# Kernel tuning notes

Hardware: AMD Instinct MI355X
Metric: run time of the kernel (lower is better)

Reference implementation:

```python
import jax, jax.numpy as jnp
import numpy as np

# physics constants (match PDELoss defaults)
RHO, CP, VZ, KT = 0.3, 1200.0, 0.5, 0.06
# Arrhenius-style soot source constants (representative RadiationPINN.soot_source_terms)
A_NUC, E_NUC = 1.0e4, 2.0e4
A_GROW, E_GROW = 5.0e3, 1.2e4
A_OX, E_OX = 1.0e5, 1.6e4

N, IN_DIM, H, OUT, N_FUELS, EMB = 262144, 12, 128, 7, 4, 8


def mlp(X, emb_rows, W1, b1, W2, b2, W3, b3, Wo, bo):
    # X: (N,4) coords; emb_rows: (N,8) fuel embedding -> T (N,1), fv (N,1), Y (N,5)
    h = jnp.concatenate([X, emb_rows], axis=-1)
    h = jnp.tanh(h @ W1 + b1)
    h = jnp.tanh(h @ W2 + b2)
    h = jnp.tanh(h @ W3 + b3)
    o = h @ Wo + bo
    T = 300.0 + 2000.0 * jax.nn.sigmoid(o[:, 0:1])
    fv = jax.nn.softplus(o[:, 1:2]) * 1e-6
    Y = jax.nn.softmax(o[:, 2:7], axis=-1)
    return T, fv, Y


def soot_sources(T, Y_prec, Y_O2, fv):
    nuc = A_NUC * Y_prec * jnp.exp(-E_NUC / T)
    grow = A_GROW * Y_prec * fv * jnp.exp(-E_GROW / T)
    ox = A_OX * Y_O2 * fv * jnp.sqrt(T) * jnp.exp(-E_OX / T)
    return nuc, grow, ox


def pde_loss(inputs, fuel_ids, W1, b1, W2, b2, W3, b3, Wo, bo, emb):
    emb_rows = emb[fuel_ids]  # (N, EMB), constant w.r.t. inputs
    params = (W1, b1, W2, b2, W3, b3, Wo, bo)

    def T_of(X):
        return mlp(X, emb_rows, *params)[0]

    def fv_of(X):
        return mlp(X, emb_rows, *params)[1]

    n = inputs.shape[0]
    Ez = jnp.zeros_like(inputs).at[:, 1].set(1.0)  # direction d/dz
    Er = jnp.zeros_like(inputs).at[:, 2].set(1.0)  # direction d/dr

    # forward-mode (Taylor) derivatives: nested jvp gives 1st and 2nd order in one pass
    dT_dz_fn = lambda X: jax.jvp(T_of, (X,), (Ez,))[1]
    dT_dz, d2T_dz2 = jax.jvp(dT_dz_fn, (inputs,), (Ez,))
    dT_dr_fn = lambda X: jax.jvp(T_of, (X,), (Er,))[1]
    dT_dr, d2T_dr2 = jax.jvp(dT_dr_fn, (inputs,), (Er,))
    _, dfv_dz = jax.jvp(fv_of, (inputs,), (Ez,))

    T, fv, Y = mlp(inputs, emb_rows, *params)
    Y_prec, Y_O2 = Y[:, 3:4], Y[:, 4:5]

    r = inputs[:, 2:3]
    r_safe = jnp.maximum(r, 1e-6)
    laplacian_r = d2T_dr2 + dT_dr / r_safe
    energy_res = RHO * CP * VZ * dT_dz - KT * laplacian_r - KT * d2T_dz2

    nuc, grow, ox = soot_sources(T, Y_prec, Y_O2, fv)
    soot_res = VZ * dfv_dz - nuc - grow + ox

    loss_energy = jnp.mean(energy_res ** 2)
    loss_soot = jnp.mean(soot_res ** 2)
    return jnp.stack([loss_energy, loss_soot, loss_energy + loss_soot])


def setup_inputs() -> dict:
    key = jax.random.key(0)
    ks = jax.random.split(key, 12)
    inputs = jax.random.uniform(ks[0], (N, 4), dtype=jnp.float32)
    fuel_ids = jax.random.randint(ks[1], (N,), 0, N_FUELS)
    s1, sh, so = 1.0 / np.sqrt(IN_DIM), 1.0 / np.sqrt(H), 1.0 / np.sqrt(H)
    return {
        "inputs": inputs,
        "fuel_ids": fuel_ids,
        "W1": jax.random.normal(ks[2], (IN_DIM, H), jnp.float32) * s1,
        "b1": jnp.zeros((H,), jnp.float32),
        "W2": jax.random.normal(ks[3], (H, H), jnp.float32) * sh,
        "b2": jnp.zeros((H,), jnp.float32),
        "W3": jax.random.normal(ks[4], (H, H), jnp.float32) * sh,
        "b3": jnp.zeros((H,), jnp.float32),
        "Wo": jax.random.normal(ks[5], (H, OUT), jnp.float32) * so,
        "bo": jnp.zeros((OUT,), jnp.float32),
        "emb": jax.random.normal(ks[6], (N_FUELS, EMB), jnp.float32) * 0.1,
    }


def reference(inputs, fuel_ids, W1, b1, W2, b2, W3, b3, Wo, bo, emb):
    return pde_loss(inputs, fuel_ids, W1, b1, W2, b2, W3, b3, Wo, bo, emb)
```

## Files before the change

kernel.cpp:

```cpp
#include <hip/hip_runtime.h>
#include <math.h>

#define NPTS 262144
#define PTS  16
#define NBLK (NPTS / PTS)
#define AP   136

typedef _Float16 f16;
typedef f16    f16x4 __attribute__((ext_vector_type(4)));
typedef f16    f16x8 __attribute__((ext_vector_type(8)));
typedef __fp16 h16x2 __attribute__((ext_vector_type(2)));
typedef __fp16 h16x4 __attribute__((ext_vector_type(4)));
typedef float  f32x4 __attribute__((ext_vector_type(4)));


__device__ __forceinline__ h16x2 pk(float a, float b) {
    return __builtin_amdgcn_cvt_pkrtz(a, b);
}
__device__ __forceinline__ f16x4 mrg(h16x2 lo, h16x2 hi) {
    h16x4 v = __builtin_shufflevector(lo, hi, 0, 1, 2, 3);
    return __builtin_bit_cast(f16x4, v);
}

__device__ __forceinline__ float fast_tanh(float z) {
    float e = __expf(2.f * z);
    return 1.f - __fdividef(2.f, e + 1.f);
}

__global__ void prep_weights(const float* __restrict__ W1, const float* __restrict__ W2,
                             const float* __restrict__ W3, const float* __restrict__ Wo,
                             const float* __restrict__ bo,
                             f16* __restrict__ wt1, f16* __restrict__ wt2,
                             f16* __restrict__ wt3, f16* __restrict__ wot,
                             float* __restrict__ bot)
{
    int tid    = blockIdx.x * blockDim.x + threadIdx.x;
    int stride = gridDim.x * blockDim.x;
    for (int i = tid; i < 128 * 32; i += stride) {
        int k = i >> 7, n = i & 127;
        wt1[n * 32 + k] = (f16)((k < 12) ? W1[k * 128 + n] : 0.f);
    }
    for (int i = tid; i < 128 * 128; i += stride) {
        int k = i >> 7, n = i & 127;
        wt2[n * 128 + k] = (f16)W2[i];
        wt3[n * 128 + k] = (f16)W3[i];
    }
    for (int i = tid; i < 16 * 128; i += stride) {
        int k = i >> 4, n = i & 15;
        wot[n * 128 + k] = (f16)((n < 7) ? Wo[k * 7 + n] : 0.f);
    }
    if (tid < 16) bot[tid] = (tid < 7) ? bo[tid] : 0.f;
}

__device__ __forceinline__ void transform_store(
    f16 (*sAct)[PTS][AP], const f32x4 acc[5], const f32x4 bv,
    int pt, int n0q)
{
    float t[4], s[4];
#pragma unroll
    for (int r = 0; r < 4; ++r) {
        float z = acc[0][r] + bv[r];
        t[r] = fast_tanh(z);
        s[r] = 1.f - t[r] * t[r];
    }
    h16x2 T[2]  = { pk(t[0], t[1]), pk(t[2], t[3]) };
    h16x2 S[2]  = { pk(s[0], s[1]), pk(s[2], s[3]) };
    h16x2 A1[2] = { pk(acc[1][0], acc[1][1]), pk(acc[1][2], acc[1][3]) };
    h16x2 A2[2] = { pk(acc[2][0], acc[2][1]), pk(acc[2][2], acc[2][3]) };
    h16x2 A3[2] = { pk(acc[3][0], acc[3][1]), pk(acc[3][2], acc[3][3]) };
    h16x2 A4[2] = { pk(acc[4][0], acc[4][1]), pk(acc[4][2], acc[4][3]) };
    h16x2 TZ[2], TZZ[2], TR[2], TRR[2];
#pragma unroll
    for (int p = 0; p < 2; ++p) {
        h16x2 n2t = -(T[p] + T[p]);
        TZ[p]  = S[p] * A1[p];
        TR[p]  = S[p] * A3[p];
        TZZ[p] = n2t * (TZ[p] * A1[p]) + S[p] * A2[p];
        TRR[p] = n2t * (TR[p] * A3[p]) + S[p] * A4[p];
    }
    *(f16x4*)&sAct[0][pt][n0q] = mrg(T[0], T[1]);
    *(f16x4*)&sAct[1][pt][n0q] = mrg(TZ[0], TZ[1]);
    *(f16x4*)&sAct[2][pt][n0q] = mrg(TZZ[0], TZZ[1]);
    *(f16x4*)&sAct[3][pt][n0q] = mrg(TR[0], TR[1]);
    *(f16x4*)&sAct[4][pt][n0q] = mrg(TRR[0], TRR[1]);
}

__device__ __forceinline__ void layer128(
    f16 (*sAct)[PTS][AP], const f16* __restrict__ Wt, const float* __restrict__ b,
    int half, int q, int m)
{
    f16x8 Bv[5][4];
#pragma unroll
    for (int c = 0; c < 5; ++c)
#pragma unroll
        for (int kt = 0; kt < 4; ++kt)
            Bv[c][kt] = *(const f16x8*)&sAct[c][m][kt * 32 + q * 8];
    __syncthreads();

    const f32x4 z4 = {0.f, 0.f, 0.f, 0.f};
#pragma unroll
    for (int ct0 = 0; ct0 < 4; ++ct0) {
        const int n0 = (half * 4 + ct0) * 16;
        const f16* wp = &Wt[(n0 + m) * 128 + q * 8];
        f16x8 A0 = *(const f16x8*)(wp);
        f16x8 A1 = *(const f16x8*)(wp + 32);
        f16x8 A2 = *(const f16x8*)(wp + 64);
        f16x8 A3 = *(const f16x8*)(wp + 96);
        f32x4 bb = *(const f32x4*)&b[n0 + q * 4];
        f32x4 acc[5];
#pragma unroll
        for (int c = 0; c < 5; ++c) acc[c] = __builtin_amdgcn_mfma_f32_16x16x32_f16(A0, Bv[c][0], z4, 0, 0, 0);
#pragma unroll
        for (int c = 0; c < 5; ++c) acc[c] = __builtin_amdgcn_mfma_f32_16x16x32_f16(A1, Bv[c][1], acc[c], 0, 0, 0);
#pragma unroll
        for (int c = 0; c < 5; ++c) acc[c] = __builtin_amdgcn_mfma_f32_16x16x32_f16(A2, Bv[c][2], acc[c], 0, 0, 0);
#pragma unroll
        for (int c = 0; c < 5; ++c) acc[c] = __builtin_amdgcn_mfma_f32_16x16x32_f16(A3, Bv[c][3], acc[c], 0, 0, 0);

        transform_store(sAct, acc, bb, m, n0 + q * 4);
    }
    __syncthreads();
}

__global__ __launch_bounds__(128, 3) void pde_main(
    const float* __restrict__ X,
    const int*   __restrict__ fid,
    const float* __restrict__ emb,
    const float* __restrict__ b1, const float* __restrict__ b2,
    const float* __restrict__ b3,
    const f16* __restrict__ Wt1, const f16* __restrict__ Wt2,
    const f16* __restrict__ Wt3, const f16* __restrict__ Wot,
    const float* __restrict__ bot,
    float* __restrict__ partials)
{
    __shared__ f32x4 smem4[5 * PTS * AP * 2 / 16];
    __shared__ float sRes[PTS][2];
    f16   (*sAct)[PTS][AP] = (f16(*)[PTS][AP])smem4;
    float (*sO)[PTS][17]   = (float(*)[PTS][17])smem4;

    const int tid  = threadIdx.x;
    const int half = tid >> 6;
    const int lane = tid & 63;
    const int q    = lane >> 4;
    const int m    = lane & 15;
    const int p0   = blockIdx.x * PTS;

    for (int idx = tid; idx < 5 * PTS * 32; idx += 128) {
        int k = idx & 31;
        int p = (idx >> 5) & (PTS - 1);
        int c = idx >> 9;
        float v = 0.f;
        if (c == 0) {
            if (k < 4)       v = X[(p0 + p) * 4 + k];
            else if (k < 12) v = emb[fid[p0 + p] * 8 + (k - 4)];
        } else if (c == 1) { v = (k == 1) ? 1.f : 0.f; }
        else if (c == 3)   { v = (k == 2) ? 1.f : 0.f; }
        sAct[c][p][k] = (f16)v;
    }
    __syncthreads();

    {
        f16x8 Bv[5];
#pragma unroll
        for (int c = 0; c < 5; ++c)
            Bv[c] = *(const f16x8*)&sAct[c][m][q * 8];
        __syncthreads();
        const f32x4 z4 = {0.f, 0.f, 0.f, 0.f};
#pragma unroll
        for (int ct0 = 0; ct0 < 4; ++ct0) {
            const int n0 = (half * 4 + ct0) * 16;
            f16x8 A0 = *(const f16x8*)&Wt1[(n0 + m) * 32 + q * 8];
            f32x4 bb = *(const f32x4*)&b1[n0 + q * 4];
            f32x4 acc[5];
#pragma unroll
            for (int c = 0; c < 5; ++c)
                acc[c] = __builtin_amdgcn_mfma_f32_16x16x32_f16(A0, Bv[c], z4, 0, 0, 0);
            transform_store(sAct, acc, bb, m, n0 + q * 4);
        }
        __syncthreads();
    }

    layer128(sAct, Wt2, b2, half, q, m);
    layer128(sAct, Wt3, b3, half, q, m);

    f16x8 Bh[5][4];
    f32x4 boq = {0.f, 0.f, 0.f, 0.f};
    if (half == 0) {
#pragma unroll
        for (int c = 0; c < 5; ++c)
#pragma unroll
            for (int kt = 0; kt < 4; ++kt)
                Bh[c][kt] = *(const f16x8*)&sAct[c][m][kt * 32 + q * 8];
        boq = *(const f32x4*)&bot[q * 4];
    }
    __syncthreads();
    if (half == 0) {
        const f16* wp = &Wot[m * 128 + q * 8];
        f16x8 A0 = *(const f16x8*)(wp);
        f16x8 A1 = *(const f16x8*)(wp + 32);
        f16x8 A2 = *(const f16x8*)(wp + 64);
        f16x8 A3 = *(const f16x8*)(wp + 96);
        const f32x4 z4 = {0.f, 0.f, 0.f, 0.f};
        f32x4 acc[5];
#pragma unroll
        for (int c = 0; c < 5; ++c) acc[c] = __builtin_amdgcn_mfma_f32_16x16x32_f16(A0, Bh[c][0], z4, 0, 0, 0);
#pragma unroll
        for (int c = 0; c < 5; ++c) acc[c] = __builtin_amdgcn_mfma_f32_16x16x32_f16(A1, Bh[c][1], acc[c], 0, 0, 0);
#pragma unroll
        for (int c = 0; c < 5; ++c) acc[c] = __builtin_amdgcn_mfma_f32_16x16x32_f16(A2, Bh[c][2], acc[c], 0, 0, 0);
#pragma unroll
        for (int c = 0; c < 5; ++c) acc[c] = __builtin_amdgcn_mfma_f32_16x16x32_f16(A3, Bh[c][3], acc[c], 0, 0, 0);
#pragma unroll
        for (int c = 0; c < 5; ++c)
#pragma unroll
            for (int r = 0; r < 4; ++r)
                sO[c][m][q * 4 + r] = acc[c][r] + ((c == 0) ? boq[r] : 0.f);
    }
    __syncthreads();

    if (tid < PTS) {
        const int pt = tid;
        float o0   = sO[0][pt][0], o1  = sO[0][pt][1];
        float o0z  = sO[1][pt][0], o1z = sO[1][pt][1];
        float o0zz = sO[2][pt][0];
        float o0r  = sO[3][pt][0];
        float o0rr = sO[4][pt][0];

        float sg  = __fdividef(1.f, 1.f + __expf(-o0));
        float T   = 300.f + 2000.f * sg;
        float sp  = sg * (1.f - sg);
        float spp = sp * (1.f - 2.f * sg);
        float Tz  = 2000.f * sp * o0z;
        float Tzz = 2000.f * (spp * o0z * o0z + sp * o0zz);
        float Tr  = 2000.f * sp * o0r;
        float Trr = 2000.f * (spp * o0r * o0r + sp * o0rr);

        float fv  = ((o1 > 20.f) ? o1 : __logf(1.f + __expf(o1))) * 1e-6f;
        float s1  = __fdividef(1.f, 1.f + __expf(-o1));
        float fvz = s1 * o1z * 1e-6f;

        float y0 = sO[0][pt][2], y1 = sO[0][pt][3], y2 = sO[0][pt][4];
        float y3 = sO[0][pt][5], y4 = sO[0][pt][6];
        float mx = fmaxf(fmaxf(fmaxf(y0, y1), fmaxf(y2, y3)), y4);
        float e0 = __expf(y0 - mx), e1 = __expf(y1 - mx), e2 = __expf(y2 - mx);
        float e3 = __expf(y3 - mx), e4 = __expf(y4 - mx);
        float inv = __fdividef(1.f, e0 + e1 + e2 + e3 + e4);
        float Yp = e3 * inv;
        float Yo = e4 * inv;

        float r   = X[(p0 + pt) * 4 + 2];
        float rs  = fmaxf(r, 1e-6f);
        float rT  = __fdividef(1.f, T);
        float lap = Trr + __fdividef(Tr, rs);
        float eres = 180.f * Tz - 0.06f * lap - 0.06f * Tzz;

        float nuc  = 1e4f * Yp * __expf(-20000.f * rT);
        float grow = 5e3f * Yp * fv * __expf(-12000.f * rT);
        float ox   = 1e5f * Yo * fv * sqrtf(T) * __expf(-16000.f * rT);
        float sres = 0.5f * fvz - nuc - grow + ox;

        sRes[pt][0] = eres * eres;
        sRes[pt][1] = sres * sres;
    }
    __syncthreads();
    if (tid == 0) {
        float se = 0.f, ss = 0.f;
#pragma unroll
        for (int p = 0; p < PTS; ++p) { se += sRes[p][0]; ss += sRes[p][1]; }
        partials[2 * blockIdx.x]     = se;
        partials[2 * blockIdx.x + 1] = ss;
    }
}

__global__ __launch_bounds__(256) void pde_finalize(
    const float* __restrict__ partials, float* __restrict__ out)
{
    __shared__ double rE[256];
    __shared__ double rS[256];
    const int tid = threadIdx.x;
    const float2* p2 = (const float2*)partials;
    double se = 0.0, ss = 0.0;
    for (int i = tid; i < NBLK; i += 256) {
        float2 v = p2[i];
        se += (double)v.x;
        ss += (double)v.y;
    }
    rE[tid] = se; rS[tid] = ss;
    __syncthreads();
    for (int s = 128; s > 0; s >>= 1) {
        if (tid < s) { rE[tid] += rE[tid + s]; rS[tid] += rS[tid + s]; }
        __syncthreads();
    }
    if (tid == 0) {
        const double invN = 1.0 / (double)NPTS;
        float le = (float)(rE[0] * invN);
        float ls = (float)(rS[0] * invN);
        out[0] = le;
        out[1] = ls;
        out[2] = le + ls;
    }
}

extern "C" void kernel_launch(void* const* d_in, const int* in_sizes, int n_in,
                              void* d_out, int out_size, void* d_ws, size_t ws_size,
                              hipStream_t stream)
{
    const float* X   = (const float*)d_in[0];
    const int*   fid = (const int*)  d_in[1];
    const float* W1  = (const float*)d_in[2];
    const float* b1  = (const float*)d_in[3];
    const float* W2  = (const float*)d_in[4];
    const float* b2  = (const float*)d_in[5];
    const float* W3  = (const float*)d_in[6];
    const float* b3  = (const float*)d_in[7];
    const float* Wo  = (const float*)d_in[8];
    const float* bo  = (const float*)d_in[9];
    const float* emb = (const float*)d_in[10];

    f16*   wt1      = (f16*)d_ws;
    f16*   wt2      = wt1 + 128 * 32;
    f16*   wt3      = wt2 + 128 * 128;
    f16*   wot      = wt3 + 128 * 128;
    float* bot      = (float*)(wot + 16 * 128);
    float* partials = bot + 16;
    float* out      = (float*)d_out;

    prep_weights<<<64, 256, 0, stream>>>(W1, W2, W3, Wo, bo, wt1, wt2, wt3, wot, bot);
    pde_main<<<NBLK, 128, 0, stream>>>(X, fid, emb, b1, b2, b3,
                                       wt1, wt2, wt3, wot, bot, partials);
    pde_finalize<<<1, 256, 0, stream>>>(partials, out);
}
```

Baseline: 286.5 us.

## Vectorize input staging, widen finalize reduction, and relax launch bounds

The per-element staging loop, which gathered X and embedding values with branches, becomes a vectorized zero-fill of the shared activation tiles. The first 16 threads then write X and embedding rows as packed f16x4 stores and set the tangent one-hot entries. The finalize kernel now uses 1024 threads instead of 256, and prep_weights launches twice as many blocks. The main kernel's launch bound drops from 3 to 2 blocks per CU, which gives the compiler more registers per thread but may lower occupancy.

After: 241.9 us (median of 2 runs). 1.18x faster.

```diff
diff --git a/kernel.cpp b/kernel.cpp
--- a/kernel.cpp
+++ b/kernel.cpp
@@ -122,7 +122,7 @@
     __syncthreads();
 }
 
-__global__ __launch_bounds__(128, 3) void pde_main(
+__global__ __launch_bounds__(128, 2) void pde_main(
     const float* __restrict__ X,
     const int*   __restrict__ fid,
     const float* __restrict__ emb,
@@ -145,17 +145,27 @@
     const int m    = lane & 15;
     const int p0   = blockIdx.x * PTS;
 
-    for (int idx = tid; idx < 5 * PTS * 32; idx += 128) {
-        int k = idx & 31;
-        int p = (idx >> 5) & (PTS - 1);
-        int c = idx >> 9;
-        float v = 0.f;
-        if (c == 0) {
-            if (k < 4)       v = X[(p0 + p) * 4 + k];
-            else if (k < 12) v = emb[fid[p0 + p] * 8 + (k - 4)];
-        } else if (c == 1) { v = (k == 1) ? 1.f : 0.f; }
-        else if (c == 3)   { v = (k == 2) ? 1.f : 0.f; }
-        sAct[c][p][k] = (f16)v;
+    {
+        const f32x4 z4 = {0.f, 0.f, 0.f, 0.f};
+        for (int i = tid; i < 5 * PTS * 4; i += 128) {
+            int row = i >> 2;
+            int seg = i & 3;
+            int c = row >> 4, p = row & 15;
+            *(f32x4*)&sAct[c][p][seg * 8] = z4;
+        }
+    }
+    __syncthreads();
+    if (tid < PTS) {
+        const int p = tid;
+        f32x4 xr = *(const f32x4*)&X[(p0 + p) * 4];
+        const float* er = &emb[fid[p0 + p] * 8];
+        f32x4 e0 = *(const f32x4*)er;
+        f32x4 e1 = *(const f32x4*)(er + 4);
+        *(f16x4*)&sAct[0][p][0] = mrg(pk(xr.x, xr.y), pk(xr.z, xr.w));
+        *(f16x4*)&sAct[0][p][4] = mrg(pk(e0.x, e0.y), pk(e0.z, e0.w));
+        *(f16x4*)&sAct[0][p][8] = mrg(pk(e1.x, e1.y), pk(e1.z, e1.w));
+        sAct[1][p][1] = (f16)1.f;
+        sAct[3][p][2] = (f16)1.f;
     }
     __syncthreads();
 
@@ -272,22 +282,22 @@
     }
 }
 
-__global__ __launch_bounds__(256) void pde_finalize(
+__global__ __launch_bounds__(1024) void pde_finalize(
     const float* __restrict__ partials, float* __restrict__ out)
 {
-    __shared__ double rE[256];
-    __shared__ double rS[256];
+    __shared__ double rE[1024];
+    __shared__ double rS[1024];
     const int tid = threadIdx.x;
     const float2* p2 = (const float2*)partials;
     double se = 0.0, ss = 0.0;
-    for (int i = tid; i < NBLK; i += 256) {
+    for (int i = tid; i < NBLK; i += 1024) {
         float2 v = p2[i];
         se += (double)v.x;
         ss += (double)v.y;
     }
     rE[tid] = se; rS[tid] = ss;
     __syncthreads();
-    for (int s = 128; s > 0; s >>= 1) {
+    for (int s = 512; s > 0; s >>= 1) {
         if (tid < s) { rE[tid] += rE[tid + s]; rS[tid] += rS[tid + s]; }
         __syncthreads();
     }
@@ -325,8 +335,8 @@
     float* partials = bot + 16;
     float* out      = (float*)d_out;
 
-    prep_weights<<<64, 256, 0, stream>>>(W1, W2, W3, Wo, bo, wt1, wt2, wt3, wot, bot);
+    prep_weights<<<128, 256, 0, stream>>>(W1, W2, W3, Wo, bo, wt1, wt2, wt3, wot, bot);
     pde_main<<<NBLK, 128, 0, stream>>>(X, fid, emb, b1, b2, b3,
                                        wt1, wt2, wt3, wot, bot, partials);
-    pde_finalize<<<1, 256, 0, stream>>>(partials, out);
-}
+    pde_finalize<<<1, 1024, 0, stream>>>(partials, out);
+}
```
